# Performance work log

Measured on AMD Instinct MI355X. Metric: run time of the kernel, lower is better.

The kernel has to match this reference:

```python
import jax, jax.numpy as jnp
import numpy as np

N_NODES = 100000   # vertices
N_EDGES = 20000    # hyperedges
NNZ = 1600000      # incidence entries (avg vertex degree 16)
D_IN = 128
D_OUT = 128


def setup_inputs() -> dict:
    key = jax.random.key(0)
    k1, k2, k3, k4, k5 = jax.random.split(key, 5)
    X = jax.random.normal(k1, (N_NODES, D_IN), dtype=jnp.float32)
    v_idx = jax.random.randint(k2, (NNZ,), 0, N_NODES)
    e_idx = jax.random.randint(k3, (NNZ,), 0, N_EDGES)
    theta_w = jax.random.normal(k4, (D_IN, D_OUT), dtype=jnp.float32) / np.sqrt(D_IN)
    theta_b = jax.random.normal(k5, (D_OUT,), dtype=jnp.float32) * 0.01
    return {"X": X, "theta_w": theta_w, "theta_b": theta_b,
            "v_idx": v_idx, "e_idx": e_idx}


def reference(X, theta_w, theta_b, v_idx, e_idx):
    # degrees (edge weights w_e = 1)
    ones = jnp.ones(v_idx.shape[0], dtype=X.dtype)
    d_v = jax.ops.segment_sum(ones, v_idx, num_segments=N_NODES)   # [N]
    d_e = jax.ops.segment_sum(ones, e_idx, num_segments=N_EDGES)   # [M]
    inv_sqrt_dv = jnp.where(d_v > 0, d_v ** -0.5, 0.0)
    inv_de = jnp.where(d_e > 0, 1.0 / d_e, 0.0)

    # theta: dense GEMM
    Xt = X @ theta_w + theta_b                                     # [N, D_OUT]

    # smoothing_with_HGNN: D_v^{-1/2} H W D_e^{-1} H^T D_v^{-1/2} Xt
    Xs = Xt * inv_sqrt_dv[:, None]                                 # [N, D_OUT]
    Ye = jax.ops.segment_sum(Xs[v_idx], e_idx, num_segments=N_EDGES)  # H^T Xs -> [M, D_OUT]
    Ye = Ye * inv_de[:, None]
    Xv = jax.ops.segment_sum(Ye[e_idx], v_idx, num_segments=N_NODES)  # H Ye -> [N, D_OUT]
    return jax.nn.relu(Xv * inv_sqrt_dv[:, None])
```

## Files before the change

### kernel.cpp

```cpp
#include <hip/hip_runtime.h>

#define N_NODES 100000
#define N_EDGES 20000
#define NNZ     1600000
#define D       128
#define DW      64

#define NB      256
#define CAP_E   8192
#define CAP_V   8192
#define SPAN_E  ((N_EDGES + NB - 1) / NB)
#define SPAN_V  ((N_NODES + NB - 1) / NB)
#define P1_CHUNK 8192
#define P1_ITER  (P1_CHUNK / 256)
#define P1_BLOCKS ((NNZ + P1_CHUNK - 1) / P1_CHUNK)

typedef __attribute__((ext_vector_type(8))) short bf16x8;
typedef __attribute__((ext_vector_type(4))) float f32x4;

__device__ __forceinline__ unsigned int pack_bf2(float lo, float hi) {
  unsigned int ul = __float_as_uint(lo), uh = __float_as_uint(hi);
  ul = (ul + 0x7FFFu + ((ul >> 16) & 1u)) >> 16;
  uh = (uh + 0x7FFFu + ((uh >> 16) & 1u)) & 0xFFFF0000u;
  return ul | uh;
}

__global__ __launch_bounds__(256) void k_prep(const float* __restrict__ W, unsigned int* __restrict__ Wtp,
                                              int* __restrict__ ce, int* __restrict__ cv,
                                              unsigned int* __restrict__ Xs, unsigned int* __restrict__ Yeb,
                                              float* __restrict__ risv) {
  int t = threadIdx.x;
  if (blockIdx.x == 0) {
    ce[t] = t * CAP_E; cv[t] = t * CAP_V;
    if (t < DW) { Xs[(size_t)N_NODES * DW + t] = 0u; Yeb[(size_t)N_EDGES * DW + t] = 0u; }
    if (t == 0) risv[N_NODES] = 0.f;
  }
  int idx = blockIdx.x * 256 + t;
  if (idx < D * DW) {
    int c = idx & 127, kp = idx >> 7;
    float lo = W[(size_t)(2 * kp) * D + c];
    float hi = W[(size_t)(2 * kp + 1) * D + c];
    Wtp[c * DW + kp] = pack_bf2(lo, hi);
  }
}

__global__ __launch_bounds__(256) void k_bin(const int* __restrict__ v_idx, const int* __restrict__ e_idx,
                                             int* __restrict__ ce, int* __restrict__ cv,
                                             unsigned int* __restrict__ Te, unsigned int* __restrict__ Tv) {
  __shared__ int he[NB], hv[NB], be[NB], bv[NB], le[NB], lv[NB];
  int t = threadIdx.x;
  he[t] = 0; hv[t] = 0; le[t] = 0; lv[t] = 0;
  __syncthreads();
  int base = blockIdx.x * P1_CHUNK;
  int v[P1_ITER], e[P1_ITER];
#pragma unroll
  for (int j = 0; j < P1_ITER; ++j) {
    int idx = base + j * 256 + t;
    if (idx < NNZ) {
      v[j] = v_idx[idx]; e[j] = e_idx[idx];
      atomicAdd(&he[e[j] / SPAN_E], 1);
      atomicAdd(&hv[v[j] / SPAN_V], 1);
    } else v[j] = -1;
  }
  __syncthreads();
  be[t] = he[t] ? atomicAdd(&ce[t], he[t]) : 0;
  bv[t] = hv[t] ? atomicAdd(&cv[t], hv[t]) : 0;
  __syncthreads();
#pragma unroll
  for (int j = 0; j < P1_ITER; ++j) {
    if (v[j] < 0) continue;
    int eb = e[j] / SPAN_E, vb = v[j] / SPAN_V;
    int se = be[eb] + atomicAdd(&le[eb], 1);
    int sv = bv[vb] + atomicAdd(&lv[vb], 1);
    if (se < (eb + 1) * CAP_E) Te[se] = ((unsigned)e[j] << 17) | (unsigned)v[j];
    if (sv < (vb + 1) * CAP_V) Tv[sv] = ((unsigned)v[j] << 15) | (unsigned)e[j];
  }
}

__global__ __launch_bounds__(256) void k_sort(const int* __restrict__ ce, const int* __restrict__ cv,
                                              unsigned int* __restrict__ Te, unsigned int* __restrict__ Tv,
                                              int* __restrict__ cnt_e, float* __restrict__ invde,
                                              int* __restrict__ starts_e,
                                              int* __restrict__ cnt_v, float* __restrict__ risv,
                                              int* __restrict__ starts_v,
                                              const float* __restrict__ X, unsigned int* __restrict__ Xs) {
  __shared__ unsigned int raw[CAP_V];
  __shared__ int hist[SPAN_V], lcur[SPAN_V], loff[SPAN_V + 1];
  __shared__ float rv[SPAN_V];
  int t = threadIdx.x;
  if (blockIdx.x < NB) {
    int b = blockIdx.x;
    int v0 = b * SPAN_V;
    int span = N_NODES - v0; if (span > SPAN_V) span = SPAN_V;
    if (span <= 0) return;
    int n = cv[b] - b * CAP_V; if (n > CAP_V) n = CAP_V; if (n < 0) n = 0;
    for (int i = t; i < n; i += 256) raw[i] = Tv[b * CAP_V + i];
    for (int i = t; i < span; i += 256) { hist[i] = 0; lcur[i] = 0; }
    __syncthreads();
    for (int i = t; i < n; i += 256) atomicAdd(&hist[(int)(raw[i] >> 15) - v0], 1);
    __syncthreads();
    if (t == 0) { int run = 0; for (int i = 0; i < span; ++i) { loff[i] = run; run += hist[i]; } loff[span] = run; }
    __syncthreads();
    for (int i = t; i < n; i += 256) {
      unsigned int p = raw[i];
      int l = (int)(p >> 15) - v0;
      int slot = loff[l] + atomicAdd(&lcur[l], 1);
      Tv[b * CAP_V + slot] = p & 0x7FFFu;
    }
    for (int i = t; i < span; i += 256) {
      int d = hist[i];
      float r = d > 0 ? rsqrtf((float)d) : 0.0f;
      cnt_v[v0 + i] = d;
      risv[v0 + i] = r;
      rv[i] = r;
      starts_v[v0 + i] = b * CAP_V + loff[i];
    }
    __syncthreads();
    int total = span * DW;
    for (int idx = t; idx < total; idx += 256) {
      int vl = idx >> 6;
      float r = rv[vl];
      size_t gp = (size_t)(v0 + vl) * DW + (idx & 63);
      float2 x = *(const float2*)(X + gp * 2);
      Xs[gp] = pack_bf2(r * x.x, r * x.y);
    }
  } else {
    int b = blockIdx.x - NB;
    int e0 = b * SPAN_E;
    int span = N_EDGES - e0; if (span > SPAN_E) span = SPAN_E;
    if (span <= 0) return;
    int n = ce[b] - b * CAP_E; if (n > CAP_E) n = CAP_E; if (n < 0) n = 0;
    for (int i = t; i < n; i += 256) raw[i] = Te[b * CAP_E + i];
    for (int i = t; i < span; i += 256) { hist[i] = 0; lcur[i] = 0; }
    __syncthreads();
    for (int i = t; i < n; i += 256) atomicAdd(&hist[(int)(raw[i] >> 17) - e0], 1);
    __syncthreads();
    if (t == 0) { int run = 0; for (int i = 0; i < span; ++i) { loff[i] = run; run += hist[i]; } loff[span] = run; }
    __syncthreads();
    for (int i = t; i < n; i += 256) {
      unsigned int p = raw[i];
      int l = (int)(p >> 17) - e0;
      int slot = loff[l] + atomicAdd(&lcur[l], 1);
      Te[b * CAP_E + slot] = p & 0x1FFFFu;
    }
    for (int i = t; i < span; i += 256) {
      int d = hist[i];
      cnt_e[e0 + i] = d;
      invde[e0 + i] = d > 0 ? 1.0f / (float)d : 0.0f;
      starts_e[e0 + i] = b * CAP_E + loff[i];
    }
  }
}

__global__ __launch_bounds__(256) void k_edge_gather(const unsigned int* __restrict__ Xs, const float* __restrict__ risv,
                              const int* __restrict__ starts_e, const int* __restrict__ cnt_e,
                              const unsigned int* __restrict__ members,
                              unsigned int* __restrict__ Qeb, float* __restrict__ qv) {
  int wv = (blockIdx.x * 256 + threadIdx.x) >> 6;
  int lane = threadIdx.x & 63;
  int g = lane >> 4, l16 = lane & 15;
  int e = wv * 4 + g;
  if (e >= N_EDGES) return;
  int beg = starts_e[e];
  int cnt = cnt_e[e];
  int maxc = cnt;
  maxc = max(maxc, __shfl_xor(maxc, 16));
  maxc = max(maxc, __shfl_xor(maxc, 32));
  float a0=0,a1=0,a2=0,a3=0,a4=0,a5=0,a6=0,a7=0,q=0.f;
  for (int i = 0; i < maxc; i += 8) {
    int vv[8];
#pragma unroll
    for (int j = 0; j < 8; ++j) {
      int idx = i + j;
      int m = (int)members[beg + idx];
      vv[j] = (idx < cnt) ? m : N_NODES;
    }
    uint4 xx[8];
#pragma unroll
    for (int j = 0; j < 8; ++j) xx[j] = *(const uint4*)(Xs + (size_t)vv[j] * DW + l16 * 4);
#pragma unroll
    for (int j = 0; j < 8; ++j) q += risv[vv[j]];
#pragma unroll
    for (int j = 0; j < 8; ++j) {
      a0 += __uint_as_float(xx[j].x << 16); a1 += __uint_as_float(xx[j].x & 0xFFFF0000u);
      a2 += __uint_as_float(xx[j].y << 16); a3 += __uint_as_float(xx[j].y & 0xFFFF0000u);
      a4 += __uint_as_float(xx[j].z << 16); a5 += __uint_as_float(xx[j].z & 0xFFFF0000u);
      a6 += __uint_as_float(xx[j].w << 16); a7 += __uint_as_float(xx[j].w & 0xFFFF0000u);
    }
  }
  uint4 o;
  o.x = pack_bf2(a0, a1); o.y = pack_bf2(a2, a3);
  o.z = pack_bf2(a4, a5); o.w = pack_bf2(a6, a7);
  *(uint4*)(Qeb + (size_t)e * DW + l16 * 4) = o;
  if (l16 == 0) qv[e] = q;
}

__global__ __launch_bounds__(256) void k_gemm(const unsigned int* __restrict__ Qeb, const float* __restrict__ qv,
                                              const unsigned int* __restrict__ Wtp, const float* __restrict__ bias,
                                              const float* __restrict__ invde, unsigned short* __restrict__ Yeb) {
  int wid = (blockIdx.x * 256 + threadIdx.x) >> 6;
  int lane = threadIdx.x & 63;
  if (wid >= N_EDGES / 16) return;
  int e0 = wid * 16;
  int lrow = lane & 15, lhalf = lane >> 4;
  const unsigned int* arow = Qeb + (size_t)(e0 + lrow) * DW + lhalf * 4;
  f32x4 acc[8];
#pragma unroll
  for (int nt = 0; nt < 8; ++nt) acc[nt] = (f32x4){0.f, 0.f, 0.f, 0.f};
#pragma unroll
  for (int kt = 0; kt < 4; ++kt) {
    bf16x8 a = *(const bf16x8*)(arow + kt * 16);
#pragma unroll
    for (int nt = 0; nt < 8; ++nt) {
      bf16x8 b = *(const bf16x8*)(Wtp + (size_t)(nt * 16 + lrow) * DW + kt * 16 + lhalf * 4);
      acc[nt] = __builtin_amdgcn_mfma_f32_16x16x32_bf16(a, b, acc[nt], 0, 0, 0);
    }
  }
#pragma unroll
  for (int r = 0; r < 4; ++r) {
    int row = e0 + lhalf * 4 + r;
    float s = invde[row], q = qv[row];
#pragma unroll
    for (int nt = 0; nt < 8; ++nt) {
      int c = nt * 16 + lrow;
      float val = s * (acc[nt][r] + q * bias[c]);
      unsigned int u = __float_as_uint(val);
      u = (u + 0x7FFFu + ((u >> 16) & 1u)) >> 16;
      Yeb[(size_t)row * D + c] = (unsigned short)u;
    }
  }
}

__global__ __launch_bounds__(256) void k_vertex_gather(const unsigned int* __restrict__ Yeb, const float* __restrict__ risv,
                                const int* __restrict__ starts_v, const int* __restrict__ cnt_v,
                                const unsigned int* __restrict__ members,
                                float* __restrict__ out) {
  int wv = (blockIdx.x * 256 + threadIdx.x) >> 6;
  int lane = threadIdx.x & 63;
  int g = lane >> 4, l16 = lane & 15;
  int v = wv * 4 + g;
  if (v >= N_NODES) return;
  int beg = starts_v[v];
  int cnt = cnt_v[v];
  int maxc = cnt;
  maxc = max(maxc, __shfl_xor(maxc, 16));
  maxc = max(maxc, __shfl_xor(maxc, 32));
  float a0=0,a1=0,a2=0,a3=0,a4=0,a5=0,a6=0,a7=0;
  for (int i = 0; i < maxc; i += 8) {
    int ee[8];
#pragma unroll
    for (int j = 0; j < 8; ++j) {
      int idx = i + j;
      int m = (int)members[beg + idx];
      ee[j] = (idx < cnt) ? m : N_EDGES;
    }
    uint4 yy[8];
#pragma unroll
    for (int j = 0; j < 8; ++j) yy[j] = *(const uint4*)(Yeb + (size_t)ee[j] * DW + l16 * 4);
#pragma unroll
    for (int j = 0; j < 8; ++j) {
      a0 += __uint_as_float(yy[j].x << 16); a1 += __uint_as_float(yy[j].x & 0xFFFF0000u);
      a2 += __uint_as_float(yy[j].y << 16); a3 += __uint_as_float(yy[j].y & 0xFFFF0000u);
      a4 += __uint_as_float(yy[j].z << 16); a5 += __uint_as_float(yy[j].z & 0xFFFF0000u);
      a6 += __uint_as_float(yy[j].w << 16); a7 += __uint_as_float(yy[j].w & 0xFFFF0000u);
    }
  }
  float s = risv[v];
  float4 o0, o1;
  o0.x = fmaxf(a0 * s, 0.f); o0.y = fmaxf(a1 * s, 0.f);
  o0.z = fmaxf(a2 * s, 0.f); o0.w = fmaxf(a3 * s, 0.f);
  o1.x = fmaxf(a4 * s, 0.f); o1.y = fmaxf(a5 * s, 0.f);
  o1.z = fmaxf(a6 * s, 0.f); o1.w = fmaxf(a7 * s, 0.f);
  float* orow = out + (size_t)v * D + l16 * 8;
  *(float4*)orow = o0;
  *(float4*)(orow + 4) = o1;
}

extern "C" void kernel_launch(void* const* d_in, const int* in_sizes, int n_in,
                              void* d_out, int out_size, void* d_ws, size_t ws_size,
                              hipStream_t stream) {
  const float* X    = (const float*)d_in[0];
  const float* W    = (const float*)d_in[1];
  const float* bias = (const float*)d_in[2];
  const int* v_idx  = (const int*)d_in[3];
  const int* e_idx  = (const int*)d_in[4];
  float* out = (float*)d_out;

  char* p = (char*)d_ws;
  auto alloc = [&](size_t bytes) { char* r = p; p += (bytes + 255) & ~(size_t)255; return r; };
  unsigned int* Te  = (unsigned int*)alloc((size_t)NB * CAP_E * 4);
  unsigned int* Tv  = (unsigned int*)alloc((size_t)NB * CAP_V * 4);
  unsigned int* Xs  = (unsigned int*)alloc((size_t)(N_NODES + 1) * DW * 4);
  unsigned int* Qeb = (unsigned int*)alloc((size_t)N_EDGES * DW * 4);
  unsigned int* Yeb = (unsigned int*)alloc((size_t)(N_EDGES + 1) * DW * 4);
  unsigned int* Wtp = (unsigned int*)alloc((size_t)D * DW * 4);
  float* qv    = (float*)alloc((size_t)N_EDGES * 4);
  float* risv  = (float*)alloc((size_t)(N_NODES + 1) * 4);
  float* invde = (float*)alloc((size_t)N_EDGES * 4);
  int* cnt_e    = (int*)alloc((size_t)N_EDGES * 4);
  int* cnt_v    = (int*)alloc((size_t)N_NODES * 4);
  int* starts_e = (int*)alloc((size_t)N_EDGES * 4);
  int* starts_v = (int*)alloc((size_t)N_NODES * 4);
  int* ce       = (int*)alloc(NB * 4);
  int* cv       = (int*)alloc(NB * 4);

  k_prep<<<(D * DW + 255) / 256, 256, 0, stream>>>(W, Wtp, ce, cv, Xs, Yeb, risv);
  k_bin<<<P1_BLOCKS, 256, 0, stream>>>(v_idx, e_idx, ce, cv, Te, Tv);
  k_sort<<<2 * NB, 256, 0, stream>>>(ce, cv, Te, Tv, cnt_e, invde, starts_e,
                                     cnt_v, risv, starts_v, X, Xs);
  k_edge_gather<<<(N_EDGES / 4 + 3) / 4, 256, 0, stream>>>(Xs, risv, starts_e, cnt_e, Te, Qeb, qv);
  k_gemm<<<(N_EDGES / 16 + 3) / 4, 256, 0, stream>>>(Qeb, qv, Wtp, bias, invde, (unsigned short*)Yeb);
  k_vertex_gather<<<(N_NODES / 4 + 3) / 4, 256, 0, stream>>>(Yeb, risv, starts_v, cnt_v, Tv, out);
}
```

Baseline: 278.6 us.

## Fuse edge gather with GEMM via LDS and parallelize bucket prefix scan

Merges the edge-gather and GEMM kernels so each block gathers 16 hyperedge rows into swizzled LDS and runs the MFMA projection directly, removing the Qeb/qv global round trip and one launch. The W repack and sentinel zeroing move into extra blocks of the sort kernel, and a tiny kernel zeroes relative bucket cursors, so k_prep goes away. The single-thread serial prefix sum in k_sort is replaced by a 256-thread Hillis-Steele scan. In exchange the GEMM now uses only 2 MFMA column tiles per wave and 1250 blocks, and the scan adds many barriers.

```diff
diff --git a/kernel.cpp b/kernel.cpp
--- a/kernel.cpp
+++ b/kernel.cpp
@@ -25,23 +25,8 @@
   return ul | uh;
 }
 
-__global__ __launch_bounds__(256) void k_prep(const float* __restrict__ W, unsigned int* __restrict__ Wtp,
-                                              int* __restrict__ ce, int* __restrict__ cv,
-                                              unsigned int* __restrict__ Xs, unsigned int* __restrict__ Yeb,
-                                              float* __restrict__ risv) {
-  int t = threadIdx.x;
-  if (blockIdx.x == 0) {
-    ce[t] = t * CAP_E; cv[t] = t * CAP_V;
-    if (t < DW) { Xs[(size_t)N_NODES * DW + t] = 0u; Yeb[(size_t)N_EDGES * DW + t] = 0u; }
-    if (t == 0) risv[N_NODES] = 0.f;
-  }
-  int idx = blockIdx.x * 256 + t;
-  if (idx < D * DW) {
-    int c = idx & 127, kp = idx >> 7;
-    float lo = W[(size_t)(2 * kp) * D + c];
-    float hi = W[(size_t)(2 * kp + 1) * D + c];
-    Wtp[c * DW + kp] = pack_bf2(lo, hi);
-  }
+__global__ void k_zero_cursors(int* __restrict__ cur) {
+  cur[threadIdx.x] = 0;
 }
 
 __global__ __launch_bounds__(256) void k_bin(const int* __restrict__ v_idx, const int* __restrict__ e_idx,
@@ -72,8 +57,8 @@
     int eb = e[j] / SPAN_E, vb = v[j] / SPAN_V;
     int se = be[eb] + atomicAdd(&le[eb], 1);
     int sv = bv[vb] + atomicAdd(&lv[vb], 1);
-    if (se < (eb + 1) * CAP_E) Te[se] = ((unsigned)e[j] << 17) | (unsigned)v[j];
-    if (sv < (vb + 1) * CAP_V) Tv[sv] = ((unsigned)v[j] << 15) | (unsigned)e[j];
+    if (se < CAP_E) Te[(size_t)eb * CAP_E + se] = ((unsigned)e[j] << 17) | (unsigned)v[j];
+    if (sv < CAP_V) Tv[(size_t)vb * CAP_V + sv] = ((unsigned)v[j] << 15) | (unsigned)e[j];
   }
 }
 
@@ -83,29 +68,60 @@
                                               int* __restrict__ starts_e,
                                               int* __restrict__ cnt_v, float* __restrict__ risv,
                                               int* __restrict__ starts_v,
-                                              const float* __restrict__ X, unsigned int* __restrict__ Xs) {
+                                              const float* __restrict__ X, unsigned int* __restrict__ Xs,
+                                              const float* __restrict__ W, unsigned int* __restrict__ Wtp,
+                                              unsigned int* __restrict__ Yeb) {
   __shared__ unsigned int raw[CAP_V];
   __shared__ int hist[SPAN_V], lcur[SPAN_V], loff[SPAN_V + 1];
+  __shared__ int sd[256];
   __shared__ float rv[SPAN_V];
   int t = threadIdx.x;
+  if (blockIdx.x >= 2 * NB) {
+    int bp = blockIdx.x - 2 * NB;
+    if (bp == 0) {
+      if (t < DW) { Xs[(size_t)N_NODES * DW + t] = 0u; Yeb[(size_t)N_EDGES * DW + t] = 0u; }
+      if (t == 0) risv[N_NODES] = 0.f;
+    }
+    int idx = bp * 256 + t;
+    if (idx < D * DW) {
+      int c = idx & 127, kp = idx >> 7;
+      float lo = W[(size_t)(2 * kp) * D + c];
+      float hi = W[(size_t)(2 * kp + 1) * D + c];
+      Wtp[c * DW + kp] = pack_bf2(lo, hi);
+    }
+    return;
+  }
   if (blockIdx.x < NB) {
     int b = blockIdx.x;
     int v0 = b * SPAN_V;
     int span = N_NODES - v0; if (span > SPAN_V) span = SPAN_V;
     if (span <= 0) return;
-    int n = cv[b] - b * CAP_V; if (n > CAP_V) n = CAP_V; if (n < 0) n = 0;
-    for (int i = t; i < n; i += 256) raw[i] = Tv[b * CAP_V + i];
+    int n = cv[b]; if (n > CAP_V) n = CAP_V; if (n < 0) n = 0;
+    for (int i = t; i < n; i += 256) raw[i] = Tv[(size_t)b * CAP_V + i];
     for (int i = t; i < span; i += 256) { hist[i] = 0; lcur[i] = 0; }
     __syncthreads();
     for (int i = t; i < n; i += 256) atomicAdd(&hist[(int)(raw[i] >> 15) - v0], 1);
     __syncthreads();
-    if (t == 0) { int run = 0; for (int i = 0; i < span; ++i) { loff[i] = run; run += hist[i]; } loff[span] = run; }
-    __syncthreads();
+    {
+      int i0 = 2 * t, i1 = 2 * t + 1;
+      int s0 = (i0 < span) ? hist[i0] : 0;
+      int s1 = (i1 < span) ? hist[i1] : 0;
+      int mysum = s0 + s1;
+      sd[t] = mysum; __syncthreads();
+      for (int off = 1; off < 256; off <<= 1) {
+        int add = (t >= off) ? sd[t - off] : 0;
+        __syncthreads(); sd[t] += add; __syncthreads();
+      }
+      int bse = sd[t] - mysum;
+      if (i0 < span) loff[i0] = bse;
+      if (i1 < span) loff[i1] = bse + s0;
+      __syncthreads();
+    }
     for (int i = t; i < n; i += 256) {
       unsigned int p = raw[i];
       int l = (int)(p >> 15) - v0;
       int slot = loff[l] + atomicAdd(&lcur[l], 1);
-      Tv[b * CAP_V + slot] = p & 0x7FFFu;
+      Tv[(size_t)b * CAP_V + slot] = p & 0x7FFFu;
     }
     for (int i = t; i < span; i += 256) {
       int d = hist[i];
@@ -129,19 +145,32 @@
     int e0 = b * SPAN_E;
     int span = N_EDGES - e0; if (span > SPAN_E) span = SPAN_E;
     if (span <= 0) return;
-    int n = ce[b] - b * CAP_E; if (n > CAP_E) n = CAP_E; if (n < 0) n = 0;
-    for (int i = t; i < n; i += 256) raw[i] = Te[b * CAP_E + i];
+    int n = ce[b]; if (n > CAP_E) n = CAP_E; if (n < 0) n = 0;
+    for (int i = t; i < n; i += 256) raw[i] = Te[(size_t)b * CAP_E + i];
     for (int i = t; i < span; i += 256) { hist[i] = 0; lcur[i] = 0; }
     __syncthreads();
     for (int i = t; i < n; i += 256) atomicAdd(&hist[(int)(raw[i] >> 17) - e0], 1);
     __syncthreads();
-    if (t == 0) { int run = 0; for (int i = 0; i < span; ++i) { loff[i] = run; run += hist[i]; } loff[span] = run; }
-    __syncthreads();
+    {
+      int i0 = 2 * t, i1 = 2 * t + 1;
+      int s0 = (i0 < span) ? hist[i0] : 0;
+      int s1 = (i1 < span) ? hist[i1] : 0;
+      int mysum = s0 + s1;
+      sd[t] = mysum; __syncthreads();
+      for (int off = 1; off < 256; off <<= 1) {
+        int add = (t >= off) ? sd[t - off] : 0;
+        __syncthreads(); sd[t] += add; __syncthreads();
+      }
+      int bse = sd[t] - mysum;
+      if (i0 < span) loff[i0] = bse;
+      if (i1 < span) loff[i1] = bse + s0;
+      __syncthreads();
+    }
     for (int i = t; i < n; i += 256) {
       unsigned int p = raw[i];
       int l = (int)(p >> 17) - e0;
       int slot = loff[l] + atomicAdd(&lcur[l], 1);
-      Te[b * CAP_E + slot] = p & 0x1FFFFu;
+      Te[(size_t)b * CAP_E + slot] = p & 0x1FFFFu;
     }
     for (int i = t; i < span; i += 256) {
       int d = hist[i];
@@ -152,15 +181,18 @@
   }
 }
 
-__global__ __launch_bounds__(256) void k_edge_gather(const unsigned int* __restrict__ Xs, const float* __restrict__ risv,
-                              const int* __restrict__ starts_e, const int* __restrict__ cnt_e,
-                              const unsigned int* __restrict__ members,
-                              unsigned int* __restrict__ Qeb, float* __restrict__ qv) {
-  int wv = (blockIdx.x * 256 + threadIdx.x) >> 6;
-  int lane = threadIdx.x & 63;
+__global__ __launch_bounds__(256) void k_eg_gemm(const unsigned int* __restrict__ Xs, const float* __restrict__ risv,
+                                                 const int* __restrict__ starts_e, const int* __restrict__ cnt_e,
+                                                 const unsigned int* __restrict__ members,
+                                                 const unsigned int* __restrict__ Wtp, const float* __restrict__ bias,
+                                                 const float* __restrict__ invde, unsigned short* __restrict__ Yeb) {
+  __shared__ unsigned int Qls[16][DW];
+  __shared__ float qls[16], ivls[16];
+  int tid = threadIdx.x;
+  int wv = tid >> 6, lane = tid & 63;
   int g = lane >> 4, l16 = lane & 15;
-  int e = wv * 4 + g;
-  if (e >= N_EDGES) return;
+  int row = wv * 4 + g;
+  int e = blockIdx.x * 16 + row;
   int beg = starts_e[e];
   int cnt = cnt_e[e];
   int maxc = cnt;
@@ -191,42 +223,34 @@
   uint4 o;
   o.x = pack_bf2(a0, a1); o.y = pack_bf2(a2, a3);
   o.z = pack_bf2(a4, a5); o.w = pack_bf2(a6, a7);
-  *(uint4*)(Qeb + (size_t)e * DW + l16 * 4) = o;
-  if (l16 == 0) qv[e] = q;
-}
-
-__global__ __launch_bounds__(256) void k_gemm(const unsigned int* __restrict__ Qeb, const float* __restrict__ qv,
-                                              const unsigned int* __restrict__ Wtp, const float* __restrict__ bias,
-                                              const float* __restrict__ invde, unsigned short* __restrict__ Yeb) {
-  int wid = (blockIdx.x * 256 + threadIdx.x) >> 6;
-  int lane = threadIdx.x & 63;
-  if (wid >= N_EDGES / 16) return;
-  int e0 = wid * 16;
-  int lrow = lane & 15, lhalf = lane >> 4;
-  const unsigned int* arow = Qeb + (size_t)(e0 + lrow) * DW + lhalf * 4;
-  f32x4 acc[8];
-#pragma unroll
-  for (int nt = 0; nt < 8; ++nt) acc[nt] = (f32x4){0.f, 0.f, 0.f, 0.f};
+  *(uint4*)&Qls[row][(l16 ^ row) * 4] = o;
+  if (l16 == 0) { qls[row] = q; ivls[row] = invde[e]; }
+  __syncthreads();
+  f32x4 acc[2];
+  acc[0] = (f32x4){0.f,0.f,0.f,0.f}; acc[1] = (f32x4){0.f,0.f,0.f,0.f};
 #pragma unroll
   for (int kt = 0; kt < 4; ++kt) {
-    bf16x8 a = *(const bf16x8*)(arow + kt * 16);
-#pragma unroll
-    for (int nt = 0; nt < 8; ++nt) {
-      bf16x8 b = *(const bf16x8*)(Wtp + (size_t)(nt * 16 + lrow) * DW + kt * 16 + lhalf * 4);
-      acc[nt] = __builtin_amdgcn_mfma_f32_16x16x32_bf16(a, b, acc[nt], 0, 0, 0);
+    int s = kt * 4 + g;
+    bf16x8 a = *(const bf16x8*)&Qls[l16][(s ^ l16) * 4];
+#pragma unroll
+    for (int n = 0; n < 2; ++n) {
+      int nt = wv * 2 + n;
+      bf16x8 b = *(const bf16x8*)(Wtp + (size_t)(nt * 16 + l16) * DW + kt * 16 + g * 4);
+      acc[n] = __builtin_amdgcn_mfma_f32_16x16x32_bf16(a, b, acc[n], 0, 0, 0);
     }
   }
 #pragma unroll
   for (int r = 0; r < 4; ++r) {
-    int row = e0 + lhalf * 4 + r;
-    float s = invde[row], q = qv[row];
-#pragma unroll
-    for (int nt = 0; nt < 8; ++nt) {
-      int c = nt * 16 + lrow;
-      float val = s * (acc[nt][r] + q * bias[c]);
+    int lrow = g * 4 + r;
+    int erow = blockIdx.x * 16 + lrow;
+    float s = ivls[lrow], qq = qls[lrow];
+#pragma unroll
+    for (int n = 0; n < 2; ++n) {
+      int c = (wv * 2 + n) * 16 + l16;
+      float val = s * (acc[n][r] + qq * bias[c]);
       unsigned int u = __float_as_uint(val);
       u = (u + 0x7FFFu + ((u >> 16) & 1u)) >> 16;
-      Yeb[(size_t)row * D + c] = (unsigned short)u;
+      Yeb[(size_t)erow * D + c] = (unsigned short)u;
     }
   }
 }
@@ -288,27 +312,25 @@
 
   char* p = (char*)d_ws;
   auto alloc = [&](size_t bytes) { char* r = p; p += (bytes + 255) & ~(size_t)255; return r; };
-  unsigned int* Te  = (unsigned int*)alloc((size_t)NB * CAP_E * 4);
-  unsigned int* Tv  = (unsigned int*)alloc((size_t)NB * CAP_V * 4);
+  unsigned int* Te  = (unsigned int*)alloc(((size_t)NB + 1) * CAP_E * 4);
+  unsigned int* Tv  = (unsigned int*)alloc(((size_t)NB + 1) * CAP_V * 4);
   unsigned int* Xs  = (unsigned int*)alloc((size_t)(N_NODES + 1) * DW * 4);
-  unsigned int* Qeb = (unsigned int*)alloc((size_t)N_EDGES * DW * 4);
   unsigned int* Yeb = (unsigned int*)alloc((size_t)(N_EDGES + 1) * DW * 4);
   unsigned int* Wtp = (unsigned int*)alloc((size_t)D * DW * 4);
-  float* qv    = (float*)alloc((size_t)N_EDGES * 4);
   float* risv  = (float*)alloc((size_t)(N_NODES + 1) * 4);
   float* invde = (float*)alloc((size_t)N_EDGES * 4);
   int* cnt_e    = (int*)alloc((size_t)N_EDGES * 4);
   int* cnt_v    = (int*)alloc((size_t)N_NODES * 4);
   int* starts_e = (int*)alloc((size_t)N_EDGES * 4);
   int* starts_v = (int*)alloc((size_t)N_NODES * 4);
-  int* ce       = (int*)alloc(NB * 4);
-  int* cv       = (int*)alloc(NB * 4);
-
-  k_prep<<<(D * DW + 255) / 256, 256, 0, stream>>>(W, Wtp, ce, cv, Xs, Yeb, risv);
+  int* cursors  = (int*)alloc((size_t)2 * NB * 4);
+  int* ce = cursors, *cv = cursors + NB;
+
+  k_zero_cursors<<<1, 2 * NB, 0, stream>>>(cursors);
   k_bin<<<P1_BLOCKS, 256, 0, stream>>>(v_idx, e_idx, ce, cv, Te, Tv);
-  k_sort<<<2 * NB, 256, 0, stream>>>(ce, cv, Te, Tv, cnt_e, invde, starts_e,
-                                     cnt_v, risv, starts_v, X, Xs);
-  k_edge_gather<<<(N_EDGES / 4 + 3) / 4, 256, 0, stream>>>(Xs, risv, starts_e, cnt_e, Te, Qeb, qv);
-  k_gemm<<<(N_EDGES / 16 + 3) / 4, 256, 0, stream>>>(Qeb, qv, Wtp, bias, invde, (unsigned short*)Yeb);
+  k_sort<<<2 * NB + 32, 256, 0, stream>>>(ce, cv, Te, Tv, cnt_e, invde, starts_e,
+                                          cnt_v, risv, starts_v, X, Xs, W, Wtp, Yeb);
+  k_eg_gemm<<<N_EDGES / 16, 256, 0, stream>>>(Xs, risv, starts_e, cnt_e, Te, Wtp, bias, invde,
+                                              (unsigned short*)Yeb);
   k_vertex_gather<<<(N_NODES / 4 + 3) / 4, 256, 0, stream>>>(Yeb, risv, starts_v, cnt_v, Tv, out);
 }
```

After: 268.2 us. 1.04x faster.
